# Kernel optimization log

Measured on AMD Instinct MI355X. Metric: run time of the kernel, lower is better.

## Reference

```python
import jax, jax.numpy as jnp
import numpy as np

HIDDEN = 1024
H2 = HIDDEN // 2
LAYERS = 2
NUM_CONDS = 4


def _lstm_dir(x, Wih, Whh, b, reverse):
    # x: (B, T, I); Wih: (4*H2, I); Whh: (4*H2, H2); b: (4*H2,)
    B = x.shape[0]
    h2 = Whh.shape[1]
    pre = jnp.einsum('bti,gi->btg', x, Wih) + b  # precompute input contribution
    pre = jnp.swapaxes(pre, 0, 1)  # (T, B, 4*H2)
    if reverse:
        pre = pre[::-1]

    def step(carry, g_in):
        h, c = carry
        g = g_in + h @ Whh.T
        i, f, gg, o = jnp.split(g, 4, axis=-1)
        c = jax.nn.sigmoid(f) * c + jax.nn.sigmoid(i) * jnp.tanh(gg)
        h = jax.nn.sigmoid(o) * jnp.tanh(c)
        return (h, c), h

    init = (jnp.zeros((B, h2), x.dtype), jnp.zeros((B, h2), x.dtype))
    _, hs = jax.lax.scan(step, init, pre)
    if reverse:
        hs = hs[::-1]
    return jnp.swapaxes(hs, 0, 1)  # (B, T, H2)


def _bilstm(x, Wih, Whh, b):
    # Wih: (L, 2, 4*H2, I) — all layers share input width since embed_dim == hidden_dim
    out = x
    for l in range(Wih.shape[0]):
        fwd = _lstm_dir(out, Wih[l, 0], Whh[l, 0], b[l, 0], False)
        bwd = _lstm_dir(out, Wih[l, 1], Whh[l, 1], b[l, 1], True)
        out = jnp.concatenate([fwd, bwd], axis=-1)
    return out


def setup_inputs() -> dict:
    key = jax.random.key(0)
    ks = jax.random.split(key, 24)
    s = 0.02
    G = 4 * H2
    inp = {
        'question_embedding': jax.random.normal(ks[0], (32, 128, 1024), jnp.float32),
        'packed_column_embedding': jax.random.normal(ks[1], (640, 8, 1024), jnp.float32),
        'gold_num': jax.random.randint(ks[2], (32,), 0, 5),
        'gold_cols': jax.random.randint(ks[3], (32, 4), 0, 20),
        'gold_ops': jax.random.randint(ks[4], (32, 4), 0, 4),
        'num_columns': 20,
        'q_Wih': jax.random.normal(ks[5], (LAYERS, 2, G, 1024), jnp.float32) * s,
        'q_Whh': jax.random.normal(ks[6], (LAYERS, 2, G, H2), jnp.float32) * s,
        'q_b': jax.random.normal(ks[7], (LAYERS, 2, G), jnp.float32) * s,
        'c_Wih': jax.random.normal(ks[8], (LAYERS, 2, G, 1024), jnp.float32) * s,
        'c_Whh': jax.random.normal(ks[9], (LAYERS, 2, G, H2), jnp.float32) * s,
        'c_b': jax.random.normal(ks[10], (LAYERS, 2, G), jnp.float32) * s,
        'col_attn_w': jax.random.normal(ks[11], (1, HIDDEN), jnp.float32) * s,
        'col_attn_b': jnp.zeros((1,), jnp.float32),
        'ob_attn_W': jax.random.normal(ks[12], (HIDDEN, HIDDEN), jnp.float32) * s,
        'ob_attn_b': jnp.zeros((HIDDEN,), jnp.float32),
        'ob_col_W': jax.random.normal(ks[13], (HIDDEN, HIDDEN), jnp.float32) * s,
        'ob_col_b': jnp.zeros((HIDDEN,), jnp.float32),
        'q_proj_W': jax.random.normal(ks[14], (HIDDEN, HIDDEN), jnp.float32) * s,
        'q_proj_b': jnp.zeros((HIDDEN,), jnp.float32),
        'out1_W': jax.random.normal(ks[15], (HIDDEN, 3 * HIDDEN), jnp.float32) * s,
        'out1_b': jnp.zeros((HIDDEN,), jnp.float32),
        'out2_W': jax.random.normal(ks[16], (2, HIDDEN), jnp.float32) * s,
        'out2_b': jnp.zeros((2,), jnp.float32),
    }
    return inp


def _forward(question_embedding, packed_column_embedding, gold_num, gold_cols,
             num_columns, q_Wih, q_Whh, q_b, c_Wih, c_Whh, c_b,
             col_attn_w, col_attn_b, ob_attn_W, ob_attn_b, ob_col_W, ob_col_b,
             q_proj_W, q_proj_b, out1_W, out1_b, out2_W, out2_b):
    dt = question_embedding.dtype
    bs, Tq, _ = question_embedding.shape
    # compute_mask: nonzero token positions
    q_mask = (jnp.abs(question_embedding).sum(-1) != 0).astype(dt)  # (B, Tq)
    c_mask = (jnp.abs(packed_column_embedding).sum(-1) != 0).astype(dt)  # (P, Tc)

    q_enc = _bilstm(question_embedding, q_Wih, q_Whh, q_b)  # (B, Tq, H)
    c_enc = _bilstm(packed_column_embedding, c_Wih, c_Whh, c_b)  # (P, Tc, H)

    # attention-pool each column name: make_weight = masked softmax over tokens
    logits = jnp.einsum('pth,oh->pt', c_enc, col_attn_w) + col_attn_b[0]
    logits = jnp.where(c_mask > 0, logits, -jnp.inf)
    w = jax.nn.softmax(logits, axis=-1)
    col_pooled = jnp.einsum('pt,pth->ph', w, c_enc)  # (P, H)
    column_hidden = col_pooled.reshape(bs, num_columns, HIDDEN)  # (B, NC, H)

    # get_observed_column_hidden (torch.no_grad): gather gold columns, zero-pad
    K = gold_cols.shape[1]
    gn = jnp.minimum(gold_num, K)
    cond_mask = (jnp.arange(K)[None, :] < gn[:, None]).astype(dt)  # (B, K)
    observed = jnp.take_along_axis(column_hidden, gold_cols[:, :, None], axis=1)  # (B, K, H)
    observed = observed * cond_mask[..., None]
    observed = jax.lax.stop_gradient(observed)
    cond_mask = jax.lax.stop_gradient(cond_mask)

    # mm_attention over question tokens
    att_key = observed @ ob_attn_W.T + ob_attn_b  # (B, K, H)
    scores = jnp.einsum('bkh,bqh->bkq', att_key, q_enc)
    scores = jnp.where(q_mask[:, None, :] > 0, scores, -jnp.inf)
    attn = jax.nn.softmax(scores, axis=-1)
    q_hidden = jnp.einsum('bkq,bqh->bkh', attn, q_enc)  # (B, K, H)

    vec = jnp.concatenate([observed @ ob_col_W.T + ob_col_b,
                           q_hidden @ q_proj_W.T + q_proj_b], axis=-1)  # (B, K, 2H)
    # broadcast concat: (B, K, Tq, 3H)
    x = jnp.concatenate([
        jnp.broadcast_to(q_enc[:, None], (bs, K, Tq, HIDDEN)),
        jnp.broadcast_to(vec[:, :, None], (bs, K, Tq, 2 * HIDDEN)),
    ], axis=-1)
    h1 = jnp.tanh(x @ out1_W.T + out1_b)
    pos = h1 @ out2_W.T + out2_b  # (B, K, Tq, 2)

    full_mask = cond_mask[:, :, None] * q_mask[:, None, :]  # (B, K, Tq)
    pos = jnp.where(full_mask[..., None] > 0, pos, -jnp.inf)
    return pos[..., 0], pos[..., 1]


def reference(question_embedding, packed_column_embedding, gold_num, gold_cols,
              gold_ops, num_columns, q_Wih, q_Whh, q_b, c_Wih, c_Whh, c_b,
              col_attn_w, col_attn_b, ob_attn_W, ob_attn_b, ob_col_W, ob_col_b,
              q_proj_W, q_proj_b, out1_W, out1_b, out2_W, out2_b):
    # gold_ops is accepted but unused by the original forward
    return _forward(question_embedding, packed_column_embedding, gold_num, gold_cols,
                    num_columns, q_Wih, q_Whh, q_b, c_Wih, c_Whh, c_b,
                    col_attn_w, col_attn_b, ob_attn_W, ob_attn_b, ob_col_W, ob_col_b,
                    q_proj_W, q_proj_b, out1_W, out1_b, out2_W, out2_b)
```

## Files before the change

### kernel.cpp

```cpp
#include <hip/hip_runtime.h>
#include <math.h>


using f32x4 = __attribute__((ext_vector_type(4))) float;
using s16x8 = __attribute__((ext_vector_type(8))) short;
typedef unsigned long long ulong_t;

#define ASYNC_COPY16(gsrc, ldst)                                               \
  __builtin_amdgcn_global_load_lds(                                            \
      (const __attribute__((address_space(1))) void*)(gsrc),                   \
      (__attribute__((address_space(3))) void*)(ldst), 16, 0, 0)

static __device__ __forceinline__ float sigm(float x) {
  return 1.0f / (1.0f + expf(-x));
}

static __device__ __forceinline__ unsigned short f2b_one(float x) {
  unsigned int u = __float_as_uint(x);
  u = (u + 0x7FFFu + ((u >> 16) & 1u)) >> 16;
  return (unsigned short)u;
}

__global__ __launch_bounds__(256) void f2b_kernel(
    const float* __restrict__ in, unsigned short* __restrict__ out, int n4)
{
  const int i = blockIdx.x * 256 + threadIdx.x;
  if (i >= n4) return;
  const float4 v = ((const float4*)in)[i];
  ushort4 r;
  r.x = f2b_one(v.x); r.y = f2b_one(v.y);
  r.z = f2b_one(v.z); r.w = f2b_one(v.w);
  ((ushort4*)out)[i] = r;
}

__global__ __launch_bounds__(256) void mask_kernel(
    const float* __restrict__ qe, const float* __restrict__ pce,
    float* __restrict__ qmask, float* __restrict__ cmask)
{
  const int w = threadIdx.x >> 6;
  const int lane = threadIdx.x & 63;
  const int row = blockIdx.x * 4 + w;
  const float* src = (row < 4096) ? (qe + (size_t)row * 1024)
                                  : (pce + (size_t)(row - 4096) * 1024);
  float s = 0.f;
#pragma unroll
  for (int j = 0; j < 16; ++j) s += fabsf(src[lane + j * 64]);
#pragma unroll
  for (int off = 32; off > 0; off >>= 1) s += __shfl_down(s, off, 64);
  if (lane == 0) {
    const float m = (s != 0.f) ? 1.f : 0.f;
    if (row < 4096) qmask[row] = m;
    else cmask[row - 4096] = m;
  }
}

__global__ __launch_bounds__(256) void mfma_gemm_kernel(
    const unsigned short* __restrict__ X, const unsigned short* __restrict__ W,
    const float* __restrict__ bias, float* __restrict__ C,
    int K, int ldx, int ldw, int k0w, int ldc, int c0)
{
  __shared__ unsigned short As[128 * 32];
  __shared__ unsigned short Bs[128 * 32];
  const int tid = threadIdx.x;
  const int w = tid >> 6;
  const int l = tid & 63;
  const int m0 = blockIdx.y * 128;
  const int n0 = blockIdx.x * 128;
  const int wm = (w >> 1) * 64;
  const int wn = (w & 1) * 64;

  const unsigned short* xg =
      X + (size_t)(m0 + w * 32 + (l >> 2)) * ldx + (l & 3) * 8;
  const unsigned short* wgp =
      W + (size_t)(n0 + w * 32 + (l >> 2)) * ldw + k0w + (l & 3) * 8;
  unsigned short* asb = As + w * 1024;
  unsigned short* bsb = Bs + w * 1024;

  const int fr = l & 15;
  const int fq = l >> 4;
  const unsigned short* aRd = As + (wm + fr) * 32 + fq * 8;
  const unsigned short* bRd = Bs + (wn + fr) * 32 + fq * 8;

  f32x4 acc[4][4];
#pragma unroll
  for (int i = 0; i < 4; ++i)
#pragma unroll
    for (int j = 0; j < 4; ++j) acc[i][j] = (f32x4){0.f, 0.f, 0.f, 0.f};

  for (int k0 = 0; k0 < K; k0 += 32) {
    ASYNC_COPY16(xg + k0, asb);
    ASYNC_COPY16(xg + (size_t)16 * ldx + k0, asb + 512);
    ASYNC_COPY16(wgp + k0, bsb);
    ASYNC_COPY16(wgp + (size_t)16 * ldw + k0, bsb + 512);
    __syncthreads();
    s16x8 a[4], b[4];
#pragma unroll
    for (int i = 0; i < 4; ++i) a[i] = *(const s16x8*)(aRd + i * 512);
#pragma unroll
    for (int j = 0; j < 4; ++j) b[j] = *(const s16x8*)(bRd + j * 512);
#pragma unroll
    for (int i = 0; i < 4; ++i)
#pragma unroll
      for (int j = 0; j < 4; ++j)
        acc[i][j] = __builtin_amdgcn_mfma_f32_16x16x32_bf16(
            a[i], b[j], acc[i][j], 0, 0, 0);
    __syncthreads();
  }

#pragma unroll
  for (int j = 0; j < 4; ++j) {
    const int col = n0 + wn + j * 16 + fr;
    const float bj = bias ? bias[col] : 0.f;
#pragma unroll
    for (int i = 0; i < 4; ++i) {
      const int row = m0 + wm + i * 16 + fq * 4;
#pragma unroll
      for (int r = 0; r < 4; ++r)
        C[(size_t)(row + r) * ldc + c0 + col] = acc[i][j][r] + bj;
    }
  }
}

__global__ __launch_bounds__(256) void gemm_kernel(
    const float* __restrict__ X, const float* __restrict__ W,
    const float* __restrict__ bias, float* __restrict__ C,
    int M, int N, int K, int ldx, int ldw, int k0w, int ldc, int c0)
{
  __shared__ float Xs[16][68];
  __shared__ float Ws[16][68];
  const int tid = threadIdx.x;
  const int m0 = blockIdx.y * 64;
  const int n0 = blockIdx.x * 64;
  const int lrow = tid >> 2;
  const int lkk = (tid & 3) << 2;
  const float* Xp = X + (size_t)(m0 + lrow) * ldx + lkk;
  const float* Wp = W + (size_t)(n0 + lrow) * ldw + k0w + lkk;
  const int tm = (tid >> 4) << 2;
  const int tn = (tid & 15) << 2;
  float acc[4][4];
#pragma unroll
  for (int i = 0; i < 4; ++i)
#pragma unroll
    for (int j = 0; j < 4; ++j) acc[i][j] = 0.f;

  for (int k0 = 0; k0 < K; k0 += 16) {
    const float4 xv = *(const float4*)(Xp + k0);
    const float4 wv = *(const float4*)(Wp + k0);
    Xs[lkk + 0][lrow] = xv.x; Xs[lkk + 1][lrow] = xv.y;
    Xs[lkk + 2][lrow] = xv.z; Xs[lkk + 3][lrow] = xv.w;
    Ws[lkk + 0][lrow] = wv.x; Ws[lkk + 1][lrow] = wv.y;
    Ws[lkk + 2][lrow] = wv.z; Ws[lkk + 3][lrow] = wv.w;
    __syncthreads();
#pragma unroll
    for (int kk = 0; kk < 16; ++kk) {
      const float4 a4 = *(const float4*)&Xs[kk][tm];
      const float4 b4 = *(const float4*)&Ws[kk][tn];
      const float av[4] = {a4.x, a4.y, a4.z, a4.w};
      const float bv[4] = {b4.x, b4.y, b4.z, b4.w};
#pragma unroll
      for (int i = 0; i < 4; ++i)
#pragma unroll
        for (int j = 0; j < 4; ++j) acc[i][j] += av[i] * bv[j];
    }
    __syncthreads();
  }
  float bvv[4] = {0.f, 0.f, 0.f, 0.f};
  if (bias) {
#pragma unroll
    for (int j = 0; j < 4; ++j) bvv[j] = bias[n0 + tn + j];
  }
#pragma unroll
  for (int i = 0; i < 4; ++i)
#pragma unroll
    for (int j = 0; j < 4; ++j)
      C[(size_t)(m0 + tm + i) * ldc + c0 + n0 + tn + j] = acc[i][j] + bvv[j];
}

template <int NT>
__global__ __launch_bounds__(512, 2) void lstm_seq_kernel(
    const float* __restrict__ pre,
    const unsigned short* __restrict__ whh,
    unsigned short* __restrict__ hbuf,
    float* __restrict__ out,
    int T, unsigned* __restrict__ bar, unsigned base)
{
  __shared__ float preS[NT][4][16][34];
  __shared__ float Tr[8][4][4][16];
  __shared__ unsigned short hS[NT * 16][36];
  __shared__ unsigned short hR[NT * 16][520];
  const int tid = threadIdx.x;
  const int v = tid >> 6;
  const int l = tid & 63;
  const int d = blockIdx.x >> 4;
  const int w = blockIdx.x & 15;
  const int bg = blockIdx.y;
  const int fr = l & 15;
  const int fq = l >> 4;
  const int ubase = w * 32;
  const int unit = ubase + v * 4 + fq;
  const int nbase = bg * (NT * 16);
  const size_t SLOT = (size_t)640 * 512;
  unsigned* ctr = bar + (d * 8 + bg) * 16;

  s16x8 afr[16];
  {
    const unsigned short* arow = whh + (size_t)d * 2048 * 512 +
        ((size_t)(fr >> 2) * 512 + ubase + v * 4 + (fr & 3)) * 512 + fq * 8;
#pragma unroll
    for (int kk = 0; kk < 16; ++kk)
      afr[kk] = *(const s16x8*)(arow + kk * 32);
  }

  float creg[NT];
#pragma unroll
  for (int i = 0; i < NT; ++i) creg[i] = 0.f;

  const int sc = tid & 7;
  const int sn = (tid >> 3) & 15;
  const int sg = tid >> 7;

  {
    const int tt0 = d ? (T - 1) : 0;
#pragma unroll
    for (int nt = 0; nt < NT; ++nt) {
      const int n = nbase + nt * 16 + sn;
      const float4 pv = *(const float4*)(
          pre + ((size_t)n * T + tt0) * 4096 + d * 2048 + sg * 512 + ubase +
          sc * 4);
      *(float4*)&preS[nt][sg][sn][sc * 4] = pv;
    }
  }
  __syncthreads();

  for (int t = 0; t < T; ++t) {
    const int tt = d ? (T - 1 - t) : t;
    const unsigned short* hr = hbuf + (size_t)((t + 1) & 1) * SLOT;
    unsigned short* hw = hbuf + (size_t)(t & 1) * SLOT;

    if (t > 0) {
      ulong_t u0[2 * NT], u1[2 * NT];
      const ulong_t* hq = (const ulong_t*)hr + (size_t)nbase * 128;
#pragma unroll
      for (int i = 0; i < 2 * NT; ++i) {
        const int cid = i * 512 + tid;
        const ulong_t* p = hq + (size_t)(cid >> 6) * 128 + (cid & 63) * 2;
        u0[i] = __hip_atomic_load(p, __ATOMIC_RELAXED,
                                  __HIP_MEMORY_SCOPE_AGENT);
        u1[i] = __hip_atomic_load(p + 1, __ATOMIC_RELAXED,
                                  __HIP_MEMORY_SCOPE_AGENT);
      }
#pragma unroll
      for (int i = 0; i < 2 * NT; ++i) {
        const int cid = i * 512 + tid;
        ulong_t* dst = (ulong_t*)&hR[cid >> 6][(cid & 63) * 8];
        dst[0] = u0[i];
        dst[1] = u1[i];
      }
    }
    __syncthreads();

#pragma unroll
    for (int nt = 0; nt < NT; ++nt) {
      f32x4 acc = (f32x4){0.f, 0.f, 0.f, 0.f};
      if (t > 0) {
        const unsigned short* bRd = &hR[nt * 16 + fr][fq * 8];
#pragma unroll
        for (int kk = 0; kk < 16; ++kk) {
          const s16x8 bv = *(const s16x8*)(bRd + kk * 32);
          acc = __builtin_amdgcn_mfma_f32_16x16x32_bf16(afr[kk], bv, acc,
                                                        0, 0, 0);
        }
      }
#pragma unroll
      for (int r = 0; r < 4; ++r) Tr[v][fq][r][fr] = acc[r];
      const int uu = v * 4 + fq;
      const float gi = Tr[v][0][fq][fr] + preS[nt][0][fr][uu];
      const float gf = Tr[v][1][fq][fr] + preS[nt][1][fr][uu];
      const float gg = Tr[v][2][fq][fr] + preS[nt][2][fr][uu];
      const float go = Tr[v][3][fq][fr] + preS[nt][3][fr][uu];
      const float cn = sigm(gf) * creg[nt] + sigm(gi) * tanhf(gg);
      const float hn = sigm(go) * tanhf(cn);
      creg[nt] = cn;
      hS[nt * 16 + fr][uu] = f2b_one(hn);
      const int n = nbase + nt * 16 + fr;
      out[((size_t)n * T + tt) * 1024 + d * 512 + unit] = hn;
    }
    __syncthreads();

    {
      const int un = tid & 7;
      const int nl = tid >> 3;
      for (int p = nl; p < NT * 16; p += 64) {
        const ulong_t val = *(const ulong_t*)&hS[p][un * 4];
        __hip_atomic_store(
            (ulong_t*)(hw + (size_t)(nbase + p) * 512 + ubase) + un, val,
            __ATOMIC_RELAXED, __HIP_MEMORY_SCOPE_AGENT);
      }
    }
    __syncthreads();

    if (tid == 0)
      __hip_atomic_fetch_add(ctr, 1u, __ATOMIC_RELAXED,
                             __HIP_MEMORY_SCOPE_AGENT);
    if (t + 1 < T) {
      const int ttn = d ? (T - 2 - t) : (t + 1);
      float4 pv[NT];
#pragma unroll
      for (int nt = 0; nt < NT; ++nt) {
        const int n = nbase + nt * 16 + sn;
        pv[nt] = *(const float4*)(
            pre + ((size_t)n * T + ttn) * 4096 + d * 2048 + sg * 512 + ubase +
            sc * 4);
      }
#pragma unroll
      for (int nt = 0; nt < NT; ++nt)
        *(float4*)&preS[nt][sg][sn][sc * 4] = pv[nt];
      if (tid == 0) {
        const unsigned target = base + (unsigned)(t + 1) * 16u;
        long spins = 0;
        while (__hip_atomic_load(ctr, __ATOMIC_RELAXED,
                                 __HIP_MEMORY_SCOPE_AGENT) < target) {
          __builtin_amdgcn_s_sleep(2);
          if (++spins > 2000000L) break;
        }
      }
    }
    __syncthreads();
  }
}

__global__ __launch_bounds__(256) void colpool_kernel(
    const float* __restrict__ cenc, const float* __restrict__ caw,
    const float* __restrict__ cab, const float* __restrict__ cmask,
    float* __restrict__ colh)
{
  __shared__ float part[8][33];
  __shared__ float wbuf[8];
  const int p = blockIdx.x;
  const int t = threadIdx.x >> 5;
  const int ln = threadIdx.x & 31;
  const float* row = cenc + ((size_t)p * 8 + t) * 1024;
  float s = 0.f;
  for (int j = ln; j < 1024; j += 32) s += row[j] * caw[j];
  part[t][ln] = s;
  __syncthreads();
  if (threadIdx.x < 8) {
    float lg = 0.f;
    for (int i = 0; i < 32; ++i) lg += part[threadIdx.x][i];
    lg += cab[0];
    wbuf[threadIdx.x] = (cmask[p * 8 + threadIdx.x] > 0.f) ? lg : -INFINITY;
  }
  __syncthreads();
  if (threadIdx.x == 0) {
    float mx = -INFINITY;
    for (int i = 0; i < 8; ++i) mx = fmaxf(mx, wbuf[i]);
    float e[8];
    float sum = 0.f;
    for (int i = 0; i < 8; ++i) { e[i] = expf(wbuf[i] - mx); sum += e[i]; }
    for (int i = 0; i < 8; ++i) wbuf[i] = e[i] / sum;
  }
  __syncthreads();
  for (int h = threadIdx.x; h < 1024; h += 256) {
    float a = 0.f;
#pragma unroll
    for (int i = 0; i < 8; ++i) a += wbuf[i] * cenc[((size_t)p * 8 + i) * 1024 + h];
    colh[(size_t)p * 1024 + h] = a;
  }
}

__global__ __launch_bounds__(256) void gather_kernel(
    const float* __restrict__ colh, const int* __restrict__ gold_num,
    const int* __restrict__ gold_cols, const int* __restrict__ ncol,
    float* __restrict__ obs)
{
  const int idx = blockIdx.x * 256 + threadIdx.x;
  const int h = idx & 1023;
  const int k = (idx >> 10) & 3;
  const int b = idx >> 12;
  int gn = gold_num[b];
  if (gn > 4) gn = 4;
  const float m = (k < gn) ? 1.f : 0.f;
  const int col = gold_cols[b * 4 + k];
  const int NC = ncol[0];
  obs[idx] = m * colh[(size_t)(b * NC + col) * 1024 + h];
}

__global__ __launch_bounds__(128) void attn_kernel(
    const float* __restrict__ akey, const float* __restrict__ qenc,
    const float* __restrict__ qmask, float* __restrict__ qhid)
{
  __shared__ float ak[1024];
  __shared__ float red[128];
  __shared__ float at[128];
  const int bk = blockIdx.x;
  const int b = bk >> 2;
  const int tid = threadIdx.x;
  for (int i = tid; i < 1024; i += 128) ak[i] = akey[(size_t)bk * 1024 + i];
  __syncthreads();
  const float* qrow = qenc + ((size_t)b * 128 + tid) * 1024;
  float s = 0.f;
  for (int hh = 0; hh < 1024; hh += 4) {
    const float4 qv = *(const float4*)(qrow + hh);
    s += ak[hh] * qv.x + ak[hh + 1] * qv.y + ak[hh + 2] * qv.z + ak[hh + 3] * qv.w;
  }
  s = (qmask[b * 128 + tid] > 0.f) ? s : -INFINITY;
  at[tid] = s;
  red[tid] = s;
  __syncthreads();
  for (int off = 64; off > 0; off >>= 1) {
    if (tid < off) red[tid] = fmaxf(red[tid], red[tid + off]);
    __syncthreads();
  }
  const float mx = red[0];
  __syncthreads();
  const float e = expf(at[tid] - mx);
  red[tid] = e;
  __syncthreads();
  for (int off = 64; off > 0; off >>= 1) {
    if (tid < off) red[tid] += red[tid + off];
    __syncthreads();
  }
  const float inv = 1.f / red[0];
  __syncthreads();
  at[tid] = e * inv;
  __syncthreads();
  for (int h = tid; h < 1024; h += 128) {
    float a = 0.f;
    for (int q = 0; q < 128; ++q)
      a += at[q] * qenc[((size_t)b * 128 + q) * 1024 + h];
    qhid[(size_t)bk * 1024 + h] = a;
  }
}

__global__ __launch_bounds__(64) void final_kernel(
    const float* __restrict__ A, const float* __restrict__ Bm,
    const float* __restrict__ w2, const float* __restrict__ b2,
    const int* __restrict__ gold_num, const float* __restrict__ qmask,
    float* __restrict__ out)
{
  const int bkq = blockIdx.x;
  const int q = bkq & 127;
  const int k = (bkq >> 7) & 3;
  const int b = bkq >> 9;
  int gn = gold_num[b];
  if (gn > 4) gn = 4;
  const bool act = (k < gn) && (qmask[b * 128 + q] > 0.f);
  const int lane = threadIdx.x;
  const int obase = (b * 4 + k) * 128 + q;
  if (!act) {
    if (lane == 0) {
      out[obase] = -1e30f;
      out[16384 + obase] = -1e30f;
    }
    return;
  }
  const float* Ar = A + ((size_t)b * 128 + q) * 1024;
  const float* Br = Bm + (size_t)(b * 4 + k) * 1024;
  float s0 = 0.f, s1 = 0.f;
  for (int o = lane; o < 1024; o += 64) {
    const float v = tanhf(Ar[o] + Br[o]);
    s0 += v * w2[o];
    s1 += v * w2[1024 + o];
  }
#pragma unroll
  for (int off = 32; off > 0; off >>= 1) {
    s0 += __shfl_down(s0, off, 64);
    s1 += __shfl_down(s1, off, 64);
  }
  if (lane == 0) {
    out[obase] = s0 + b2[0];
    out[16384 + obase] = s1 + b2[1];
  }
}

extern "C" void kernel_launch(void* const* d_in, const int* in_sizes, int n_in,
                              void* d_out, int out_size, void* d_ws, size_t ws_size,
                              hipStream_t stream)
{
  const float* qe      = (const float*)d_in[0];
  const float* pce     = (const float*)d_in[1];
  const int* gold_num  = (const int*)d_in[2];
  const int* gold_cols = (const int*)d_in[3];
  const int* ncol      = (const int*)d_in[5];
  const float* q_Wih   = (const float*)d_in[6];
  const float* q_Whh   = (const float*)d_in[7];
  const float* q_b     = (const float*)d_in[8];
  const float* c_Wih   = (const float*)d_in[9];
  const float* c_Whh   = (const float*)d_in[10];
  const float* c_b     = (const float*)d_in[11];
  const float* caw     = (const float*)d_in[12];
  const float* cab     = (const float*)d_in[13];
  const float* obaW    = (const float*)d_in[14];
  const float* obab    = (const float*)d_in[15];
  const float* obcW    = (const float*)d_in[16];
  const float* obcb    = (const float*)d_in[17];
  const float* qpW     = (const float*)d_in[18];
  const float* qpb     = (const float*)d_in[19];
  const float* o1W     = (const float*)d_in[20];
  const float* o1b     = (const float*)d_in[21];
  const float* o2W     = (const float*)d_in[22];
  const float* o2b     = (const float*)d_in[23];
  float* outp = (float*)d_out;

  float* ws = (float*)d_ws;
  size_t off = 0;
  float* pre  = ws + off; off += 640UL * 8 * 4096;
  float* bufA = ws + off; off += 640UL * 8 * 1024;
  float* bufB = ws + off; off += 640UL * 8 * 1024;
  float* colh = ws + off; off += 640UL * 1024;
  float* qmask = ws + off; off += 4096;
  float* cmask = ws + off; off += 5120;
  float* obs  = ws + off; off += 131072;
  float* akey = ws + off; off += 131072;
  float* qhid = ws + off; off += 131072;
  float* vec  = ws + off; off += 262144;
  float* Bm   = ws + off; off += 131072;
  unsigned short* xb = (unsigned short*)(ws + off); off += 2621440;
  unsigned short* wb = (unsigned short*)(ws + off); off += 2097152;
  unsigned short* whhq = (unsigned short*)(ws + off); off += 2097152;
  unsigned short* whhc = (unsigned short*)(ws + off); off += 2097152;
  unsigned short* hbuf = (unsigned short*)(ws + off); off += 327680;
  unsigned* bar = (unsigned*)(ws + off); off += 256;
  float* Amat = pre;

  const dim3 blk(256);
  auto cvt = [&](const float* src, unsigned short* dst, int n) {
    hipLaunchKernelGGL(f2b_kernel, dim3((n / 4 + 255) / 256), blk, 0, stream,
                       src, dst, n / 4);
  };

  hipMemsetAsync(bar, 0, 1024, stream);

  hipLaunchKernelGGL(mask_kernel, dim3(2304), blk, 0, stream, qe, pce, qmask, cmask);

  cvt(q_Whh, whhq, 4194304);
  cvt(c_Whh, whhc, 4194304);

  for (int l = 0; l < 2; ++l) {
    const float* xin = (l == 0) ? pce : bufA;
    float* enc = (l == 0) ? bufA : bufB;
    cvt(xin, xb, 5242880);
    cvt(c_Wih + (size_t)l * 4194304, wb, 4194304);
    hipLaunchKernelGGL(mfma_gemm_kernel, dim3(4096 / 128, 5120 / 128), blk, 0,
                       stream, xb, wb, c_b + l * 4096, pre,
                       1024, 1024, 1024, 0, 4096, 0);
    hipLaunchKernelGGL((lstm_seq_kernel<5>), dim3(32, 8), dim3(512), 0, stream,
                       pre, whhc + (size_t)l * 2 * 2048 * 512, hbuf, enc,
                       8, bar, (unsigned)(l * 128));
  }
  hipLaunchKernelGGL(colpool_kernel, dim3(640), blk, 0, stream,
                     bufB, caw, cab, cmask, colh);
  hipLaunchKernelGGL(gather_kernel, dim3(512), blk, 0, stream,
                     colh, gold_num, gold_cols, ncol, obs);

  for (int l = 0; l < 2; ++l) {
    const float* xin = (l == 0) ? qe : bufA;
    float* enc = (l == 0) ? bufA : bufB;
    cvt(xin, xb, 4194304);
    cvt(q_Wih + (size_t)l * 4194304, wb, 4194304);
    hipLaunchKernelGGL(mfma_gemm_kernel, dim3(4096 / 128, 4096 / 128), blk, 0,
                       stream, xb, wb, q_b + l * 4096, pre,
                       1024, 1024, 1024, 0, 4096, 0);
    hipLaunchKernelGGL((lstm_seq_kernel<2>), dim3(32, 1), dim3(512), 0, stream,
                       pre, whhq + (size_t)l * 2 * 2048 * 512, hbuf, enc,
                       128, bar, (unsigned)(256 + l * 2048));
  }
  const float* qenc = bufB;

  hipLaunchKernelGGL(gemm_kernel, dim3(16, 2), blk, 0, stream,
                     obs, obaW, obab, akey, 128, 1024, 1024, 1024, 1024, 0, 1024, 0);
  hipLaunchKernelGGL(attn_kernel, dim3(128), dim3(128), 0, stream,
                     akey, qenc, qmask, qhid);
  hipLaunchKernelGGL(gemm_kernel, dim3(16, 2), blk, 0, stream,
                     obs, obcW, obcb, vec, 128, 1024, 1024, 1024, 1024, 0, 2048, 0);
  hipLaunchKernelGGL(gemm_kernel, dim3(16, 2), blk, 0, stream,
                     qhid, qpW, qpb, vec, 128, 1024, 1024, 1024, 1024, 0, 2048, 1024);
  cvt(qenc, xb, 4194304);
  cvt(o1W, wb, 3145728);
  hipLaunchKernelGGL(mfma_gemm_kernel, dim3(1024 / 128, 4096 / 128), blk, 0,
                     stream, xb, wb, o1b, Amat, 1024, 1024, 3072, 0, 1024, 0);
  hipLaunchKernelGGL(gemm_kernel, dim3(16, 2), blk, 0, stream,
                     vec, o1W, nullptr, Bm, 128, 1024, 2048, 2048, 3072, 1024, 1024, 0);
  hipLaunchKernelGGL(final_kernel, dim3(16384), dim3(64), 0, stream,
                     Amat, Bm, o2W, o2b, gold_num, qmask, outp);
}
```

Baseline: 1.982 ms.

## Replace per-step counter barrier with sentinel-polled quad-buffered hidden state

The persistent LSTM recurrence kernel no longer uses a global atomic counter barrier every timestep. Each direction now gets four hidden-state slots that are pre-filled with a NaN sentinel, and readers spin until no sentinel halfwords remain. Only one counter barrier is kept at startup, and the pre-activation prefetch and output stores are moved to overlap with compute and fewer block barriers. This removes the per-step grid-wide synchronisation latency, at the cost of more polling traffic, a larger buffer, and reliance on relaxed-atomic ordering for correctness.

```diff
diff --git a/kernel.cpp b/kernel.cpp
--- a/kernel.cpp
+++ b/kernel.cpp
@@ -20,6 +20,12 @@
   u = (u + 0x7FFFu + ((u >> 16) & 1u)) >> 16;
   return (unsigned short)u;
 }
+
+static __device__ __forceinline__ bool haszero16(ulong_t x) {
+  return ((x - 0x0001000100010001ull) & ~x & 0x8000800080008000ull) != 0ull;
+}
+
+#define SENT64 0x7FC07FC07FC07FC0ull
 
 __global__ __launch_bounds__(256) void f2b_kernel(
     const float* __restrict__ in, unsigned short* __restrict__ out, int n4)
@@ -201,6 +207,7 @@
   const int nbase = bg * (NT * 16);
   const size_t SLOT = (size_t)640 * 512;
   unsigned* ctr = bar + (d * 8 + bg) * 16;
+  unsigned short* sl = hbuf + (size_t)d * 4 * SLOT;
 
   s16x8 afr[16];
   {
@@ -219,6 +226,12 @@
   const int sn = (tid >> 3) & 15;
   const int sg = tid >> 7;
 
+  for (int s = 0; s < 4; ++s) {
+    ulong_t* cb = (ulong_t*)(sl + (size_t)s * SLOT + (size_t)nbase * 512 + ubase);
+    for (int i = tid; i < NT * 16 * 8; i += 512)
+      __hip_atomic_store(cb + (size_t)(i >> 3) * 128 + (i & 7), SENT64,
+                         __ATOMIC_RELAXED, __HIP_MEMORY_SCOPE_AGENT);
+  }
   {
     const int tt0 = d ? (T - 1) : 0;
 #pragma unroll
@@ -231,33 +244,78 @@
     }
   }
   __syncthreads();
-
+  if (tid == 0) {
+    __hip_atomic_fetch_add(ctr, 1u, __ATOMIC_RELAXED,
+                           __HIP_MEMORY_SCOPE_AGENT);
+    const unsigned target = base + 16u;
+    long spins = 0;
+    while (__hip_atomic_load(ctr, __ATOMIC_RELAXED,
+                             __HIP_MEMORY_SCOPE_AGENT) < target) {
+      __builtin_amdgcn_s_sleep(1);
+      if (++spins > 2000000L) break;
+    }
+  }
+  __syncthreads();
+
+  float hnreg[NT];
   for (int t = 0; t < T; ++t) {
     const int tt = d ? (T - 1 - t) : t;
-    const unsigned short* hr = hbuf + (size_t)((t + 1) & 1) * SLOT;
-    unsigned short* hw = hbuf + (size_t)(t & 1) * SLOT;
-
+    const unsigned short* rd = sl + (size_t)((t + 3) & 3) * SLOT;
+    unsigned short* wr = sl + (size_t)(t & 3) * SLOT;
+
+    ulong_t u[4 * NT];
     if (t > 0) {
-      ulong_t u0[2 * NT], u1[2 * NT];
-      const ulong_t* hq = (const ulong_t*)hr + (size_t)nbase * 128;
-#pragma unroll
-      for (int i = 0; i < 2 * NT; ++i) {
-        const int cid = i * 512 + tid;
-        const ulong_t* p = hq + (size_t)(cid >> 6) * 128 + (cid & 63) * 2;
-        u0[i] = __hip_atomic_load(p, __ATOMIC_RELAXED,
-                                  __HIP_MEMORY_SCOPE_AGENT);
-        u1[i] = __hip_atomic_load(p + 1, __ATOMIC_RELAXED,
-                                  __HIP_MEMORY_SCOPE_AGENT);
+      const ulong_t* hq = (const ulong_t*)rd + (size_t)nbase * 128;
+      bool ok = false;
+      int it = 0;
+      while (!ok && it < 1000000) {
+#pragma unroll
+        for (int i = 0; i < 2 * NT; ++i) {
+          const int cid = i * 512 + tid;
+          const ulong_t* p = hq + (size_t)(cid >> 6) * 128 + (cid & 63) * 2;
+          u[2 * i] = __hip_atomic_load(p, __ATOMIC_RELAXED,
+                                       __HIP_MEMORY_SCOPE_AGENT);
+          u[2 * i + 1] = __hip_atomic_load(p + 1, __ATOMIC_RELAXED,
+                                           __HIP_MEMORY_SCOPE_AGENT);
+        }
+        bool bad = false;
+#pragma unroll
+        for (int i = 0; i < 4 * NT; ++i)
+          if (haszero16(u[i] ^ SENT64)) bad = true;
+        ok = !bad;
+        ++it;
+        if (!ok && it > 8) __builtin_amdgcn_s_sleep(1);
       }
 #pragma unroll
       for (int i = 0; i < 2 * NT; ++i) {
         const int cid = i * 512 + tid;
         ulong_t* dst = (ulong_t*)&hR[cid >> 6][(cid & 63) * 8];
-        dst[0] = u0[i];
-        dst[1] = u1[i];
+        dst[0] = u[2 * i];
+        dst[1] = u[2 * i + 1];
       }
     }
-    __syncthreads();
+    asm volatile("" ::: "memory");
+    {
+      ulong_t* cb = (ulong_t*)(sl + (size_t)((t + 1) & 3) * SLOT +
+                               (size_t)nbase * 512 + ubase);
+      for (int i = tid; i < NT * 16 * 8; i += 512)
+        __hip_atomic_store(cb + (size_t)(i >> 3) * 128 + (i & 7), SENT64,
+                           __ATOMIC_RELAXED, __HIP_MEMORY_SCOPE_AGENT);
+    }
+    float4 pv[NT];
+    if (t + 1 < T) {
+      const int ttn = d ? (T - 2 - t) : (t + 1);
+#pragma unroll
+      for (int nt = 0; nt < NT; ++nt) {
+        const int n = nbase + nt * 16 + sn;
+        pv[nt] = *(const float4*)(
+            pre + ((size_t)n * T + ttn) * 4096 + d * 2048 + sg * 512 + ubase +
+            sc * 4);
+      }
+    }
+    asm volatile("s_waitcnt lgkmcnt(0)" ::: "memory");
+    __builtin_amdgcn_s_barrier();
+    __builtin_amdgcn_sched_barrier(0);
 
 #pragma unroll
     for (int nt = 0; nt < NT; ++nt) {
@@ -281,51 +339,34 @@
       const float cn = sigm(gf) * creg[nt] + sigm(gi) * tanhf(gg);
       const float hn = sigm(go) * tanhf(cn);
       creg[nt] = cn;
+      hnreg[nt] = hn;
       hS[nt * 16 + fr][uu] = f2b_one(hn);
-      const int n = nbase + nt * 16 + fr;
-      out[((size_t)n * T + tt) * 1024 + d * 512 + unit] = hn;
-    }
-    __syncthreads();
-
+    }
+    asm volatile("s_waitcnt lgkmcnt(0)" ::: "memory");
+    __builtin_amdgcn_s_barrier();
+    __builtin_amdgcn_sched_barrier(0);
+
+    if (t + 1 < T) {
+#pragma unroll
+      for (int nt = 0; nt < NT; ++nt)
+        *(float4*)&preS[nt][sg][sn][sc * 4] = pv[nt];
+    }
+    asm volatile("s_waitcnt vmcnt(0)" ::: "memory");
     {
       const int un = tid & 7;
       const int nl = tid >> 3;
       for (int p = nl; p < NT * 16; p += 64) {
         const ulong_t val = *(const ulong_t*)&hS[p][un * 4];
         __hip_atomic_store(
-            (ulong_t*)(hw + (size_t)(nbase + p) * 512 + ubase) + un, val,
+            (ulong_t*)(wr + (size_t)(nbase + p) * 512 + ubase) + un, val,
             __ATOMIC_RELAXED, __HIP_MEMORY_SCOPE_AGENT);
       }
     }
-    __syncthreads();
-
-    if (tid == 0)
-      __hip_atomic_fetch_add(ctr, 1u, __ATOMIC_RELAXED,
-                             __HIP_MEMORY_SCOPE_AGENT);
-    if (t + 1 < T) {
-      const int ttn = d ? (T - 2 - t) : (t + 1);
-      float4 pv[NT];
-#pragma unroll
-      for (int nt = 0; nt < NT; ++nt) {
-        const int n = nbase + nt * 16 + sn;
-        pv[nt] = *(const float4*)(
-            pre + ((size_t)n * T + ttn) * 4096 + d * 2048 + sg * 512 + ubase +
-            sc * 4);
-      }
-#pragma unroll
-      for (int nt = 0; nt < NT; ++nt)
-        *(float4*)&preS[nt][sg][sn][sc * 4] = pv[nt];
-      if (tid == 0) {
-        const unsigned target = base + (unsigned)(t + 1) * 16u;
-        long spins = 0;
-        while (__hip_atomic_load(ctr, __ATOMIC_RELAXED,
-                                 __HIP_MEMORY_SCOPE_AGENT) < target) {
-          __builtin_amdgcn_s_sleep(2);
-          if (++spins > 2000000L) break;
-        }
-      }
-    }
-    __syncthreads();
+#pragma unroll
+    for (int nt = 0; nt < NT; ++nt) {
+      const int n = nbase + nt * 16 + fr;
+      out[((size_t)n * T + tt) * 1024 + d * 512 + unit] = hnreg[nt];
+    }
   }
 }
 
@@ -519,7 +560,7 @@
   unsigned short* wb = (unsigned short*)(ws + off); off += 2097152;
   unsigned short* whhq = (unsigned short*)(ws + off); off += 2097152;
   unsigned short* whhc = (unsigned short*)(ws + off); off += 2097152;
-  unsigned short* hbuf = (unsigned short*)(ws + off); off += 327680;
+  unsigned short* hbuf = (unsigned short*)(ws + off); off += 1310720;
   unsigned* bar = (unsigned*)(ws + off); off += 256;
   float* Amat = pre;
 
@@ -546,7 +587,7 @@
                        1024, 1024, 1024, 0, 4096, 0);
     hipLaunchKernelGGL((lstm_seq_kernel<5>), dim3(32, 8), dim3(512), 0, stream,
                        pre, whhc + (size_t)l * 2 * 2048 * 512, hbuf, enc,
-                       8, bar, (unsigned)(l * 128));
+                       8, bar, (unsigned)(l * 16));
   }
   hipLaunchKernelGGL(colpool_kernel, dim3(640), blk, 0, stream,
                      bufB, caw, cab, cmask, colh);
@@ -563,7 +604,7 @@
                        1024, 1024, 1024, 0, 4096, 0);
     hipLaunchKernelGGL((lstm_seq_kernel<2>), dim3(32, 1), dim3(512), 0, stream,
                        pre, whhq + (size_t)l * 2 * 2048 * 512, hbuf, enc,
-                       128, bar, (unsigned)(256 + l * 2048));
+                       128, bar, (unsigned)(32 + l * 16));
   }
   const float* qenc = bufB;
 
```

New measurement: 2.162 ms. +9.1%, slower.
